# Optimization experiments

Measured on AMD Instinct MI355X. Metric: run time of the kernel, lower is better.

The kernel has to match this reference:

```python
import jax, jax.numpy as jnp
import numpy as np

B, C, H, W, N = 32, 256, 56, 56, 1024


def setup_inputs() -> dict:
    key = jax.random.key(0)
    k1, k2, k3, k4 = jax.random.split(key, 4)
    x = jax.random.normal(k1, (B, C, H, W), dtype=jnp.float32)
    W_s = jax.random.normal(k2, (N, H, W), dtype=jnp.float32)
    W_d = jax.random.normal(k3, (N, C, 1, 1), dtype=jnp.float32)
    W_b = jax.random.normal(k4, (1, N), dtype=jnp.float32)
    return {"x": x, "W_s": W_s, "W_d": W_d, "W_b": W_b}


def reference(x, W_s, W_d, W_b):
    # Original: out = einsum('bchw,nhw->bnchw'); per-neuron 1x1 conv with W_d[n]
    # (C -> 1 channel); sum over (c,h,w); add bias. Mathematically:
    #   out[b,n] = sum_{c,h,w} x[b,c,h,w] * W_s[n,h,w] * W_d[n,c] + W_b[0,n]
    # Computed without materializing the (B,N,C,H,W) blow-up:
    y = jnp.einsum('bchw,nhw->bnc', x, W_s)          # spatial contraction
    out = jnp.einsum('bnc,nc->bn', y, W_d[:, :, 0, 0])  # channel contraction
    return out + W_b
```

## Files before the change

kernel.cpp:

```cpp
#include <hip/hip_runtime.h>
#include <stdint.h>


#define K_DIM 3136
#define N_DIM 1024
#define C_DIM 256
#define B_DIM 32
#define M_DIM 8192
#define X_ELEMS (M_DIM * K_DIM)
#define WS_ELEMS (N_DIM * K_DIM)

typedef __attribute__((ext_vector_type(8))) short short8v;
typedef __attribute__((ext_vector_type(4))) float f32x4;

__device__ __forceinline__ short f2bf(float f) {
  union { float f; unsigned u; } v; v.f = f;
  unsigned r = v.u + 0x7FFFu + ((v.u >> 16) & 1u);
  return (short)(r >> 16);
}

__device__ __forceinline__ void async16(const void* g, void* l) {
  __builtin_amdgcn_global_load_lds(
      (const __attribute__((address_space(1))) unsigned int*)g,
      (__attribute__((address_space(3))) unsigned int*)l, 16, 0, 0);
}

#define XBLK (X_ELEMS / 2048)
#define CVBLK ((X_ELEMS + WS_ELEMS) / 2048)
__global__ __launch_bounds__(256) void convert_bf16_bias(
    const float* __restrict__ x, const float* __restrict__ Ws,
    const float* __restrict__ Wb, short* __restrict__ dst,
    float* __restrict__ out) {
  int bid = blockIdx.x;
  if (bid >= CVBLK) {
    int i = (bid - CVBLK) * 256 + threadIdx.x;
    out[i] = Wb[i & (N_DIM - 1)];
    return;
  }
  const float* src;
  short* d;
  size_t base;
  if (bid < XBLK) {
    src = x; d = dst; base = (size_t)bid * 2048;
  } else {
    src = Ws; d = dst + X_ELEMS; base = (size_t)(bid - XBLK) * 2048;
  }
  size_t i = base + threadIdx.x * 8;
  f32x4 v0 = __builtin_nontemporal_load((const f32x4*)(src + i));
  f32x4 v1 = __builtin_nontemporal_load((const f32x4*)(src + i) + 1);
  short8v s;
  s[0] = f2bf(v0.x); s[1] = f2bf(v0.y); s[2] = f2bf(v0.z); s[3] = f2bf(v0.w);
  s[4] = f2bf(v1.x); s[5] = f2bf(v1.y); s[6] = f2bf(v1.z); s[7] = f2bf(v1.w);
  *(short8v*)(d + i) = s;
}

__global__ __launch_bounds__(256, 3) void gemm_fused(
    const short* __restrict__ Abf, const short* __restrict__ Bbf,
    const float* __restrict__ Wd, float* __restrict__ out) {
  __shared__ __align__(16) short As[256 * 64];
  __shared__ __align__(16) short Bs[128 * 64];

  const int bid = blockIdx.x;
  const int mt = bid & 31;
  const int nt = (bid >> 5) & 7;
  const int z = bid >> 8;
  const int kt0 = (z == 0) ? 0 : (17 + (z - 1) * 16);
  const int ktn = (z == 0) ? 17 : 16;

  const int t = threadIdx.x;
  const int lane = t & 63;
  const int wv = t >> 6;
  const int r = lane & 15;
  const int q = lane >> 4;
  const int wm = wv >> 1, wn = wv & 1;

  const int rr = lane >> 3;
  const int k8 = (lane & 7) ^ rr;
  const short* Aw = Abf + (size_t)(mt * 256 + wv * 64 + rr) * K_DIM + k8 * 8 + kt0 * 64;
  const short* Bw = Bbf + (size_t)(nt * 128 + wv * 32 + rr) * K_DIM + k8 * 8 + kt0 * 64;
  char* AsB = (char*)As + wv * 8192;
  char* BsB = (char*)Bs + wv * 4096;

  f32x4 acc[8][4];
#pragma unroll
  for (int i = 0; i < 8; ++i)
#pragma unroll
    for (int j = 0; j < 4; ++j) acc[i][j] = (f32x4)0.0f;

  for (int kt = 0; kt < ktn; ++kt) {
    __syncthreads();
#pragma unroll
    for (int p = 0; p < 8; ++p)
      async16(Aw + (size_t)p * 8 * K_DIM + kt * 64, AsB + p * 1024);
#pragma unroll
    for (int p = 0; p < 4; ++p)
      async16(Bw + (size_t)p * 8 * K_DIM + kt * 64, BsB + p * 1024);
    __syncthreads();

#pragma unroll
    for (int ks = 0; ks < 2; ++ks) {
      const int xo = ((ks * 4 + q) ^ (r & 7)) * 16;
      short8v b[4];
#pragma unroll
      for (int j = 0; j < 4; ++j)
        b[j] = *(const short8v*)((const char*)Bs + (64 * wn + 16 * j + r) * 128 + xo);
#pragma unroll
      for (int i = 0; i < 8; ++i) {
        short8v a =
            *(const short8v*)((const char*)As + (128 * wm + 16 * i + r) * 128 + xo);
#pragma unroll
        for (int j = 0; j < 4; ++j)
          acc[i][j] = __builtin_amdgcn_mfma_f32_16x16x32_bf16(a, b[j],
                                                              acc[i][j], 0, 0, 0);
      }
    }
  }

#pragma unroll
  for (int j = 0; j < 4; ++j) {
    const int n_g = nt * 128 + 64 * wn + 16 * j + r;
    float p = 0.0f;
#pragma unroll
    for (int i = 0; i < 8; ++i) {
      const int c_l = 128 * wm + 16 * i + 4 * q;
      const float4 wd = *(const float4*)(Wd + (size_t)n_g * C_DIM + c_l);
      p += acc[i][j].x * wd.x + acc[i][j].y * wd.y + acc[i][j].z * wd.z +
           acc[i][j].w * wd.w;
    }
    p += __shfl_xor(p, 16, 64);
    p += __shfl_xor(p, 32, 64);
    if (q == 0) atomicAdd(&out[(size_t)mt * N_DIM + n_g], p);
  }
}

extern "C" void kernel_launch(void* const* d_in, const int* in_sizes, int n_in,
                              void* d_out, int out_size, void* d_ws, size_t ws_size,
                              hipStream_t stream) {
  const float* x = (const float*)d_in[0];
  const float* Ws = (const float*)d_in[1];
  const float* Wd = (const float*)d_in[2];
  const float* Wb = (const float*)d_in[3];
  float* out = (float*)d_out;
  short* xbf = (short*)d_ws;

  convert_bf16_bias<<<dim3(CVBLK + 128), dim3(256), 0, stream>>>(x, Ws, Wb, xbf, out);
  gemm_fused<<<dim3(32 * 8 * 3), dim3(256), 0, stream>>>(xbf, xbf + X_ELEMS, Wd, out);
}
```

Measured before the change: 214.6 us.

## Warp-specialize GEMM with producer/consumer LDS ring buffer, drop split-K

```diff
diff --git a/kernel.cpp b/kernel.cpp
--- a/kernel.cpp
+++ b/kernel.cpp
@@ -9,6 +9,8 @@
 #define M_DIM 8192
 #define X_ELEMS (M_DIM * K_DIM)
 #define WS_ELEMS (N_DIM * K_DIM)
+#define SLOT_BYTES 49152
+#define NSLOT 3
 
 typedef __attribute__((ext_vector_type(8))) short short8v;
 typedef __attribute__((ext_vector_type(4))) float f32x4;
@@ -25,8 +27,8 @@
       (__attribute__((address_space(3))) unsigned int*)l, 16, 0, 0);
 }
 
-#define XBLK (X_ELEMS / 2048)
-#define CVBLK ((X_ELEMS + WS_ELEMS) / 2048)
+#define XBLK (X_ELEMS / 4096)
+#define CVBLK ((X_ELEMS + WS_ELEMS) / 4096)
 __global__ __launch_bounds__(256) void convert_bf16_bias(
     const float* __restrict__ x, const float* __restrict__ Ws,
     const float* __restrict__ Wb, short* __restrict__ dst,
@@ -41,84 +43,114 @@
   short* d;
   size_t base;
   if (bid < XBLK) {
-    src = x; d = dst; base = (size_t)bid * 2048;
+    src = x; d = dst; base = (size_t)bid * 4096;
   } else {
-    src = Ws; d = dst + X_ELEMS; base = (size_t)(bid - XBLK) * 2048;
+    src = Ws; d = dst + X_ELEMS; base = (size_t)(bid - XBLK) * 4096;
   }
-  size_t i = base + threadIdx.x * 8;
-  f32x4 v0 = __builtin_nontemporal_load((const f32x4*)(src + i));
-  f32x4 v1 = __builtin_nontemporal_load((const f32x4*)(src + i) + 1);
-  short8v s;
-  s[0] = f2bf(v0.x); s[1] = f2bf(v0.y); s[2] = f2bf(v0.z); s[3] = f2bf(v0.w);
-  s[4] = f2bf(v1.x); s[5] = f2bf(v1.y); s[6] = f2bf(v1.z); s[7] = f2bf(v1.w);
-  *(short8v*)(d + i) = s;
+#pragma unroll
+  for (int h = 0; h < 2; ++h) {
+    size_t i = base + threadIdx.x * 8 + h * 2048;
+    f32x4 v0 = __builtin_nontemporal_load((const f32x4*)(src + i));
+    f32x4 v1 = __builtin_nontemporal_load((const f32x4*)(src + i) + 1);
+    short8v s;
+    s[0] = f2bf(v0.x); s[1] = f2bf(v0.y); s[2] = f2bf(v0.z); s[3] = f2bf(v0.w);
+    s[4] = f2bf(v1.x); s[5] = f2bf(v1.y); s[6] = f2bf(v1.z); s[7] = f2bf(v1.w);
+    *(short8v*)(d + i) = s;
+  }
 }
 
-__global__ __launch_bounds__(256, 3) void gemm_fused(
+__global__ __launch_bounds__(512, 2) void gemm_fused(
     const short* __restrict__ Abf, const short* __restrict__ Bbf,
     const float* __restrict__ Wd, float* __restrict__ out) {
-  __shared__ __align__(16) short As[256 * 64];
-  __shared__ __align__(16) short Bs[128 * 64];
+  __shared__ __align__(16) char ring[NSLOT * SLOT_BYTES];
+  __shared__ int prod_cnt[NSLOT];
+  __shared__ int cons_cnt[NSLOT];
 
   const int bid = blockIdx.x;
   const int mt = bid & 31;
-  const int nt = (bid >> 5) & 7;
-  const int z = bid >> 8;
-  const int kt0 = (z == 0) ? 0 : (17 + (z - 1) * 16);
-  const int ktn = (z == 0) ? 17 : 16;
+  const int nt = bid >> 5;
+  const int KT = 49;
 
   const int t = threadIdx.x;
   const int lane = t & 63;
   const int wv = t >> 6;
-  const int r = lane & 15;
+  const int lr = lane & 15;
   const int q = lane >> 4;
+
+  if (t < NSLOT) { prod_cnt[t] = 0; cons_cnt[t] = 0; }
+  __syncthreads();
+
+  if (wv >= 4) {
+    const int p = wv - 4;
+    const int rr = lane >> 3;
+    const int k8 = (lane & 7) ^ rr;
+    const short* Aw = Abf + (size_t)(mt * 256 + p * 64 + rr) * K_DIM + k8 * 8;
+    const short* Bw = Bbf + (size_t)(nt * 128 + p * 32 + rr) * K_DIM + k8 * 8;
+    for (int kt = 0; kt < KT; ++kt) {
+      const int s = kt % NSLOT;
+      const int r = kt / NSLOT;
+      if (r > 0) {
+        volatile int* cc = cons_cnt;
+        while (cc[s] < 4 * r) {}
+      }
+      char* As_s = ring + s * SLOT_BYTES;
+      char* Bs_s = As_s + 32768;
+#pragma unroll
+      for (int i = 0; i < 8; ++i)
+        async16(Aw + (size_t)i * 8 * K_DIM + kt * 64,
+                As_s + p * 8192 + i * 1024);
+#pragma unroll
+      for (int i = 0; i < 4; ++i)
+        async16(Bw + (size_t)i * 8 * K_DIM + kt * 64,
+                Bs_s + p * 4096 + i * 1024);
+      __builtin_amdgcn_s_waitcnt(0);
+      __builtin_amdgcn_sched_barrier(0);
+      if (lane == 0) atomicAdd(&prod_cnt[s], 1);
+    }
+    return;
+  }
+
   const int wm = wv >> 1, wn = wv & 1;
-
-  const int rr = lane >> 3;
-  const int k8 = (lane & 7) ^ rr;
-  const short* Aw = Abf + (size_t)(mt * 256 + wv * 64 + rr) * K_DIM + k8 * 8 + kt0 * 64;
-  const short* Bw = Bbf + (size_t)(nt * 128 + wv * 32 + rr) * K_DIM + k8 * 8 + kt0 * 64;
-  char* AsB = (char*)As + wv * 8192;
-  char* BsB = (char*)Bs + wv * 4096;
-
   f32x4 acc[8][4];
 #pragma unroll
   for (int i = 0; i < 8; ++i)
 #pragma unroll
     for (int j = 0; j < 4; ++j) acc[i][j] = (f32x4)0.0f;
 
-  for (int kt = 0; kt < ktn; ++kt) {
-    __syncthreads();
-#pragma unroll
-    for (int p = 0; p < 8; ++p)
-      async16(Aw + (size_t)p * 8 * K_DIM + kt * 64, AsB + p * 1024);
-#pragma unroll
-    for (int p = 0; p < 4; ++p)
-      async16(Bw + (size_t)p * 8 * K_DIM + kt * 64, BsB + p * 1024);
-    __syncthreads();
-
+  for (int kt = 0; kt < KT; ++kt) {
+    const int s = kt % NSLOT;
+    const int r = kt / NSLOT;
+    {
+      volatile int* pc = prod_cnt;
+      while (pc[s] < 4 * (r + 1)) {}
+    }
+    __builtin_amdgcn_sched_barrier(0);
+    const char* As_s = ring + s * SLOT_BYTES;
+    const char* Bs_s = As_s + 32768;
 #pragma unroll
     for (int ks = 0; ks < 2; ++ks) {
-      const int xo = ((ks * 4 + q) ^ (r & 7)) * 16;
+      const int xo = ((ks * 4 + q) ^ (lr & 7)) * 16;
       short8v b[4];
 #pragma unroll
       for (int j = 0; j < 4; ++j)
-        b[j] = *(const short8v*)((const char*)Bs + (64 * wn + 16 * j + r) * 128 + xo);
+        b[j] = *(const short8v*)(Bs_s + (64 * wn + 16 * j + lr) * 128 + xo);
 #pragma unroll
       for (int i = 0; i < 8; ++i) {
-        short8v a =
-            *(const short8v*)((const char*)As + (128 * wm + 16 * i + r) * 128 + xo);
+        short8v a = *(const short8v*)(As_s + (128 * wm + 16 * i + lr) * 128 + xo);
 #pragma unroll
         for (int j = 0; j < 4; ++j)
           acc[i][j] = __builtin_amdgcn_mfma_f32_16x16x32_bf16(a, b[j],
                                                               acc[i][j], 0, 0, 0);
       }
     }
+    __builtin_amdgcn_s_waitcnt(0);
+    __builtin_amdgcn_sched_barrier(0);
+    if (lane == 0) atomicAdd(&cons_cnt[s], 1);
   }
 
 #pragma unroll
   for (int j = 0; j < 4; ++j) {
-    const int n_g = nt * 128 + 64 * wn + 16 * j + r;
+    const int n_g = nt * 128 + 64 * wn + 16 * j + lr;
     float p = 0.0f;
 #pragma unroll
     for (int i = 0; i < 8; ++i) {
@@ -144,5 +176,5 @@
   short* xbf = (short*)d_ws;
 
   convert_bf16_bias<<<dim3(CVBLK + 128), dim3(256), 0, stream>>>(x, Ws, Wb, xbf, out);
-  gemm_fused<<<dim3(32 * 8 * 3), dim3(256), 0, stream>>>(xbf, xbf + X_ELEMS, Wd, out);
+  gemm_fused<<<dim3(32 * 8), dim3(512), 0, stream>>>(xbf, xbf + X_ELEMS, Wd, out);
 }
```

Result: no change. 211.1 us (-1.6%).

## Enlarge GEMM tile to 256x256 with 8 waves and 2-way split-K

Applied to the files above, without the earlier changes.

```diff
diff --git a/kernel.cpp b/kernel.cpp
--- a/kernel.cpp
+++ b/kernel.cpp
@@ -25,8 +25,8 @@
       (__attribute__((address_space(3))) unsigned int*)l, 16, 0, 0);
 }
 
-#define XBLK (X_ELEMS / 2048)
-#define CVBLK ((X_ELEMS + WS_ELEMS) / 2048)
+#define XBLK (X_ELEMS / 4096)
+#define CVBLK ((X_ELEMS + WS_ELEMS) / 4096)
 __global__ __launch_bounds__(256) void convert_bf16_bias(
     const float* __restrict__ x, const float* __restrict__ Ws,
     const float* __restrict__ Wb, short* __restrict__ dst,
@@ -41,45 +41,48 @@
   short* d;
   size_t base;
   if (bid < XBLK) {
-    src = x; d = dst; base = (size_t)bid * 2048;
+    src = x; d = dst; base = (size_t)bid * 4096;
   } else {
-    src = Ws; d = dst + X_ELEMS; base = (size_t)(bid - XBLK) * 2048;
+    src = Ws; d = dst + X_ELEMS; base = (size_t)(bid - XBLK) * 4096;
   }
-  size_t i = base + threadIdx.x * 8;
-  f32x4 v0 = __builtin_nontemporal_load((const f32x4*)(src + i));
-  f32x4 v1 = __builtin_nontemporal_load((const f32x4*)(src + i) + 1);
-  short8v s;
-  s[0] = f2bf(v0.x); s[1] = f2bf(v0.y); s[2] = f2bf(v0.z); s[3] = f2bf(v0.w);
-  s[4] = f2bf(v1.x); s[5] = f2bf(v1.y); s[6] = f2bf(v1.z); s[7] = f2bf(v1.w);
-  *(short8v*)(d + i) = s;
+#pragma unroll
+  for (int h = 0; h < 2; ++h) {
+    size_t i = base + threadIdx.x * 8 + h * 2048;
+    f32x4 v0 = __builtin_nontemporal_load((const f32x4*)(src + i));
+    f32x4 v1 = __builtin_nontemporal_load((const f32x4*)(src + i) + 1);
+    short8v s;
+    s[0] = f2bf(v0.x); s[1] = f2bf(v0.y); s[2] = f2bf(v0.z); s[3] = f2bf(v0.w);
+    s[4] = f2bf(v1.x); s[5] = f2bf(v1.y); s[6] = f2bf(v1.z); s[7] = f2bf(v1.w);
+    *(short8v*)(d + i) = s;
+  }
 }
 
-__global__ __launch_bounds__(256, 3) void gemm_fused(
+__global__ __launch_bounds__(512, 2) void gemm_fused(
     const short* __restrict__ Abf, const short* __restrict__ Bbf,
     const float* __restrict__ Wd, float* __restrict__ out) {
   __shared__ __align__(16) short As[256 * 64];
-  __shared__ __align__(16) short Bs[128 * 64];
+  __shared__ __align__(16) short Bs[256 * 64];
 
   const int bid = blockIdx.x;
   const int mt = bid & 31;
-  const int nt = (bid >> 5) & 7;
-  const int z = bid >> 8;
-  const int kt0 = (z == 0) ? 0 : (17 + (z - 1) * 16);
-  const int ktn = (z == 0) ? 17 : 16;
+  const int nt = (bid >> 5) & 3;
+  const int z = bid >> 7;
+  const int kt0 = z * 25;
+  const int ktn = z ? 24 : 25;
 
   const int t = threadIdx.x;
   const int lane = t & 63;
   const int wv = t >> 6;
-  const int r = lane & 15;
+  const int lr = lane & 15;
   const int q = lane >> 4;
-  const int wm = wv >> 1, wn = wv & 1;
+  const int wm = wv >> 2, wn = wv & 3;
 
   const int rr = lane >> 3;
   const int k8 = (lane & 7) ^ rr;
-  const short* Aw = Abf + (size_t)(mt * 256 + wv * 64 + rr) * K_DIM + k8 * 8 + kt0 * 64;
-  const short* Bw = Bbf + (size_t)(nt * 128 + wv * 32 + rr) * K_DIM + k8 * 8 + kt0 * 64;
-  char* AsB = (char*)As + wv * 8192;
-  char* BsB = (char*)Bs + wv * 4096;
+  const short* Aw = Abf + (size_t)(mt * 256 + wv * 32 + rr) * K_DIM + k8 * 8 + kt0 * 64;
+  const short* Bw = Bbf + (size_t)(nt * 256 + wv * 32 + rr) * K_DIM + k8 * 8 + kt0 * 64;
+  char* AsW = (char*)As + wv * 4096;
+  char* BsW = (char*)Bs + wv * 4096;
 
   f32x4 acc[8][4];
 #pragma unroll
@@ -90,24 +93,23 @@
   for (int kt = 0; kt < ktn; ++kt) {
     __syncthreads();
 #pragma unroll
-    for (int p = 0; p < 8; ++p)
-      async16(Aw + (size_t)p * 8 * K_DIM + kt * 64, AsB + p * 1024);
-#pragma unroll
-    for (int p = 0; p < 4; ++p)
-      async16(Bw + (size_t)p * 8 * K_DIM + kt * 64, BsB + p * 1024);
+    for (int p = 0; p < 4; ++p) {
+      async16(Aw + (size_t)p * 8 * K_DIM + kt * 64, AsW + p * 1024);
+      async16(Bw + (size_t)p * 8 * K_DIM + kt * 64, BsW + p * 1024);
+    }
     __syncthreads();
 
 #pragma unroll
     for (int ks = 0; ks < 2; ++ks) {
-      const int xo = ((ks * 4 + q) ^ (r & 7)) * 16;
+      const int xo = ((ks * 4 + q) ^ (lr & 7)) * 16;
       short8v b[4];
 #pragma unroll
       for (int j = 0; j < 4; ++j)
-        b[j] = *(const short8v*)((const char*)Bs + (64 * wn + 16 * j + r) * 128 + xo);
+        b[j] = *(const short8v*)((const char*)Bs + (64 * wn + 16 * j + lr) * 128 + xo);
 #pragma unroll
       for (int i = 0; i < 8; ++i) {
         short8v a =
-            *(const short8v*)((const char*)As + (128 * wm + 16 * i + r) * 128 + xo);
+            *(const short8v*)((const char*)As + (128 * wm + 16 * i + lr) * 128 + xo);
 #pragma unroll
         for (int j = 0; j < 4; ++j)
           acc[i][j] = __builtin_amdgcn_mfma_f32_16x16x32_bf16(a, b[j],
@@ -118,7 +120,7 @@
 
 #pragma unroll
   for (int j = 0; j < 4; ++j) {
-    const int n_g = nt * 128 + 64 * wn + 16 * j + r;
+    const int n_g = nt * 256 + 64 * wn + 16 * j + lr;
     float p = 0.0f;
 #pragma unroll
     for (int i = 0; i < 8; ++i) {
@@ -144,5 +146,5 @@
   short* xbf = (short*)d_ws;
 
   convert_bf16_bias<<<dim3(CVBLK + 128), dim3(256), 0, stream>>>(x, Ws, Wb, xbf, out);
-  gemm_fused<<<dim3(32 * 8 * 3), dim3(256), 0, stream>>>(xbf, xbf + X_ELEMS, Wd, out);
+  gemm_fused<<<dim3(32 * 4 * 2), dim3(512), 0, stream>>>(xbf, xbf + X_ELEMS, Wd, out);
 }
```

Result: slower. 220.4 us (+2.7%).
